# Kernel tuning notes

Hardware: AMD Instinct MI355X
Metric: run time of the kernel (lower is better)

## Reference

```python
import jax, jax.numpy as jnp
import numpy as np

R, N, E, F, D, A = 3, 50000, 800000, 128, 128, 64
EPS = 1e-5


def setup_inputs() -> dict:
    key = jax.random.key(0)
    ks = jax.random.split(key, 8)
    s = 0.05
    feat = jax.random.normal(ks[0], (N, F), jnp.float32)
    src = jax.random.randint(ks[1], (R, E), 0, N)
    dst = jax.random.randint(ks[2], (R, E), 0, N)
    W0 = jax.random.normal(ks[3], (R, F, D), jnp.float32) * s
    b0 = jnp.zeros((R, D), jnp.float32)
    W1 = jax.random.normal(ks[4], (R, D, D), jnp.float32) * s
    b1 = jnp.zeros((R, D), jnp.float32)
    ln_g = jnp.ones((R, D), jnp.float32)   # per-relation MessageTransform LayerNorm (shared across its 2 layers)
    ln_b = jnp.zeros((R, D), jnp.float32)
    LN_g = jnp.ones((D,), jnp.float32)     # final PROVGEM layer_norm
    LN_b = jnp.zeros((D,), jnp.float32)
    Wa1 = jax.random.normal(ks[5], (R, D, A), jnp.float32) * s  # semantic attention proj
    Wa2 = jax.random.normal(ks[6], (R, A), jnp.float32) * s     # semantic attention score vec
    return dict(feat=feat, src=src, dst=dst, W0=W0, b0=b0, W1=W1, b1=b1,
                ln_g=ln_g, ln_b=ln_b, LN_g=LN_g, LN_b=LN_b, Wa1=Wa1, Wa2=Wa2)


def _ln(x, g, b):
    mu = jnp.mean(x, axis=-1, keepdims=True)
    var = jnp.mean(jnp.square(x - mu), axis=-1, keepdims=True)
    return (x - mu) * jax.lax.rsqrt(var + EPS) * g + b


def _mean_agg(feat, src_r, dst_r):
    # copy_u + mean: gather source feats along edges, segment-mean into dst nodes
    msg = feat[src_r]                                            # [E, F]
    ssum = jax.ops.segment_sum(msg, dst_r, num_segments=N)       # [N, F]
    deg = jax.ops.segment_sum(jnp.ones((E,), feat.dtype), dst_r, num_segments=N)
    return ssum / jnp.maximum(deg, 1.0)[:, None]                 # 0 for zero-degree nodes


def reference(feat, src, dst, W0, b0, W1, b1, ln_g, ln_b, LN_g, LN_b, Wa1, Wa2):
    # per-relation aggregation (loop over small fixed R=3)
    neigh = jnp.stack([_mean_agg(feat, src[r], dst[r]) for r in range(R)])  # [R, N, F]
    h = feat[None, :, :] + neigh                                            # residual add
    x = jnp.einsum('rnf,rfd->rnd', h, W0) + b0[:, None, :]
    x = jax.nn.relu(_ln(x, ln_g[:, None, :], ln_b[:, None, :]))
    x = jnp.einsum('rnd,rde->rne', x, W1) + b1[:, None, :]
    x = jax.nn.relu(_ln(x, ln_g[:, None, :], ln_b[:, None, :]))
    # final LayerNorm over [R, N, D]
    h = _ln(x, LN_g, LN_b)
    # semantic attention over relations
    e = jnp.einsum('rna,ra->rn', jnp.tanh(jnp.einsum('rnd,rda->rna', h, Wa1)), Wa2)
    attn = jax.nn.softmax(e, axis=0)                                        # softmax over relations
    return jnp.einsum('rn,rnd->nd', attn, h)                                # [N, D]
```

## Files before the change

kernel.cpp:

```cpp
#include <hip/hip_runtime.h>

#define RR 3
#define NN 50000
#define EE 800000
#define FF 128
#define DD 128
#define AA 64
#define EPSF 1e-5f
#define RN (RR * NN)
#define RE (RR * EE)
#define NTPR ((NN + 127) / 128)
#define NBK (RR * NTPR)
#define ECHUNK 8192
#define NEBLK ((RE + ECHUNK - 1) / ECHUNK)
#define NTILES (NN / 16)

typedef __attribute__((ext_vector_type(8))) short bf16x8;
typedef __attribute__((ext_vector_type(4))) float f32x4;
typedef __attribute__((ext_vector_type(2))) float f32x2;

__device__ __forceinline__ short f2bs(float x) {
    union { float f; unsigned u; } v; v.f = x;
    unsigned rr = (v.u + 0x7fffu + ((v.u >> 16) & 1u)) >> 16;
    return (short)(rr & 0xffffu);
}

__device__ __forceinline__ float bs2f_lo(int p) {
    union { unsigned u; float f; } v; v.u = (unsigned)p << 16; return v.f;
}
__device__ __forceinline__ float bs2f_hi(int p) {
    union { unsigned u; float f; } v; v.u = (unsigned)p & 0xffff0000u; return v.f;
}

__device__ __forceinline__ int rel_of(long e) {
    return (e >= 2L * EE) ? 2 : ((e >= (long)EE) ? 1 : 0);
}

__device__ __forceinline__ float ftanh(float x) {
    float a = __expf(2.0f * fabsf(x));
    return copysignf(1.0f - 2.0f / (a + 1.0f), x);
}

__global__ __launch_bounds__(256)
void feat2both(const float* __restrict__ feat, short* __restrict__ featb,
               int* __restrict__ featq) {
    int gid = blockIdx.x * blockDim.x + threadIdx.x;
    if (gid >= NN * 16) return;
    f32x4 a = ((const f32x4*)feat)[2 * gid];
    f32x4 b = ((const f32x4*)feat)[2 * gid + 1];
    bf16x8 o;
    o[0] = f2bs(a.x); o[1] = f2bs(a.y); o[2] = f2bs(a.z); o[3] = f2bs(a.w);
    o[4] = f2bs(b.x); o[5] = f2bs(b.y); o[6] = f2bs(b.z); o[7] = f2bs(b.w);
    ((bf16x8*)featb)[gid] = o;
    int lo = 0, hi = 0;
    lo = __builtin_amdgcn_cvt_pk_fp8_f32(a.x, a.y, lo, false);
    lo = __builtin_amdgcn_cvt_pk_fp8_f32(a.z, a.w, lo, true);
    hi = __builtin_amdgcn_cvt_pk_fp8_f32(b.x, b.y, hi, false);
    hi = __builtin_amdgcn_cvt_pk_fp8_f32(b.z, b.w, hi, true);
    int2 pk; pk.x = lo; pk.y = hi;
    ((int2*)featq)[gid] = pk;
}

__global__ __launch_bounds__(256)
void count_kernel(const int* __restrict__ dst, int* __restrict__ bcnt) {
    __shared__ int hist[NBK];
    for (int i = threadIdx.x; i < NBK; i += 256) hist[i] = 0;
    __syncthreads();
    long ebase = (long)blockIdx.x * ECHUNK;
    for (int i = threadIdx.x; i < ECHUNK; i += 256) {
        long e = ebase + i;
        if (e < RE)
            atomicAdd(&hist[rel_of(e) * NTPR + (dst[e] >> 7)], 1);
    }
    __syncthreads();
    for (int i = threadIdx.x; i < NBK; i += 256) {
        int v = hist[i];
        if (v) atomicAdd(&bcnt[i], v);
    }
}

__global__ __launch_bounds__(256)
void bscan_kernel(const int* __restrict__ bcnt, int* __restrict__ bstart,
                  int* __restrict__ boff) {
    __shared__ int sm[256];
    int t = threadIdx.x;
    int loc[5];
    int s = 0;
    #pragma unroll
    for (int i = 0; i < 5; ++i) {
        int idx = t * 5 + i;
        int v = (idx < NBK) ? bcnt[idx] : 0;
        loc[i] = v; s += v;
    }
    sm[t] = s;
    __syncthreads();
    for (int d = 1; d < 256; d <<= 1) {
        int u = (t >= d) ? sm[t - d] : 0;
        __syncthreads();
        sm[t] += u;
        __syncthreads();
    }
    int run = sm[t] - s;
    #pragma unroll
    for (int i = 0; i < 5; ++i) {
        int idx = t * 5 + i;
        if (idx < NBK) { bstart[idx] = run; boff[idx] = run; run += loc[i]; }
    }
}

__global__ __launch_bounds__(256)
void bscatterA(const int* __restrict__ src, const int* __restrict__ dst,
               int* __restrict__ boff, unsigned* __restrict__ bpair) {
    __shared__ int hist[NBK];
    __shared__ int base[NBK];
    for (int i = threadIdx.x; i < NBK; i += 256) hist[i] = 0;
    __syncthreads();
    long ebase = (long)blockIdx.x * ECHUNK;
    for (int i = threadIdx.x; i < ECHUNK; i += 256) {
        long e = ebase + i;
        if (e < RE)
            atomicAdd(&hist[rel_of(e) * NTPR + (dst[e] >> 7)], 1);
    }
    __syncthreads();
    for (int i = threadIdx.x; i < NBK; i += 256) {
        int v = hist[i];
        base[i] = v ? atomicAdd(&boff[i], v) : 0;
    }
    __syncthreads();
    for (int i = threadIdx.x; i < ECHUNK; i += 256) {
        long e = ebase + i;
        if (e < RE) {
            int r = rel_of(e);
            int d = dst[e];
            int b = r * NTPR + (d >> 7);
            int pos = atomicAdd(&base[b], 1);
            bpair[pos] = ((unsigned)(d & 127) << 16) | (unsigned)src[e];
        }
    }
}

__global__ __launch_bounds__(256)
void scatterB(const unsigned* __restrict__ bpair, const int* __restrict__ bstart,
              const int* __restrict__ bcnt,
              int* __restrict__ off, int* __restrict__ cnt,
              int* __restrict__ csr) {
    __shared__ int hist[128];
    __shared__ int pre[128];
    __shared__ int base[128];
    int b = blockIdx.x;
    int r = b / NTPR, tile = b - r * NTPR;
    const int t = threadIdx.x;
    if (t < 128) hist[t] = 0;
    __syncthreads();
    int start = bstart[b], end = start + bcnt[b];
    for (int i = start + t; i < end; i += 256)
        atomicAdd(&hist[bpair[i] >> 16], 1);
    __syncthreads();
    if (t < 128) pre[t] = hist[t];
    __syncthreads();
    for (int d = 1; d < 128; d <<= 1) {
        int v = (t < 128 && t >= d) ? pre[t - d] : 0;
        __syncthreads();
        if (t < 128) pre[t] += v;
        __syncthreads();
    }
    if (t < 128) {
        int excl = pre[t] - hist[t];
        base[t] = start + excl;
        int nloc = tile * 128 + t;
        if (nloc < NN) {
            off[r * NN + nloc] = start + excl;
            cnt[r * NN + nloc] = hist[t];
        }
        hist[t] = 0;
    }
    __syncthreads();
    for (int i = start + t; i < end; i += 256) {
        unsigned p = bpair[i];
        int d = (int)(p >> 16);
        int rank = atomicAdd(&hist[d], 1);
        csr[base[d] + rank] = (int)(p & 0xFFFFu);
    }
}

__global__ __launch_bounds__(256)
void gather_kernel(const short* __restrict__ featb,
                   const int* __restrict__ featq,
                   const int* __restrict__ csr,
                   const int* __restrict__ off,
                   const int* __restrict__ cnt,
                   short* __restrict__ ssumb) {
    int gid = blockIdx.x * blockDim.x + threadIdx.x;
    int w = gid >> 6, lane = gid & 63;
    if (w >= RN) return;
    int c = cnt[w];
    int start = off[w];
    int end = start + c;
    const unsigned short* q = (const unsigned short*)featq;
    float ax0 = 0.f, ay0 = 0.f, ax1 = 0.f, ay1 = 0.f;
    float ax2 = 0.f, ay2 = 0.f, ax3 = 0.f, ay3 = 0.f;
    float ax4 = 0.f, ay4 = 0.f, ax5 = 0.f, ay5 = 0.f;
    float ax6 = 0.f, ay6 = 0.f, ax7 = 0.f, ay7 = 0.f;
    int j = start;
    for (; j + 7 < end; j += 8) {
        int s0 = csr[j + 0], s1 = csr[j + 1], s2 = csr[j + 2], s3 = csr[j + 3];
        int s4 = csr[j + 4], s5 = csr[j + 5], s6 = csr[j + 6], s7 = csr[j + 7];
        int v0 = q[(size_t)s0 * 64 + lane];
        int v1 = q[(size_t)s1 * 64 + lane];
        int v2 = q[(size_t)s2 * 64 + lane];
        int v3 = q[(size_t)s3 * 64 + lane];
        int v4 = q[(size_t)s4 * 64 + lane];
        int v5 = q[(size_t)s5 * 64 + lane];
        int v6 = q[(size_t)s6 * 64 + lane];
        int v7 = q[(size_t)s7 * 64 + lane];
        f32x2 f0 = __builtin_amdgcn_cvt_pk_f32_fp8(v0, false);
        f32x2 f1 = __builtin_amdgcn_cvt_pk_f32_fp8(v1, false);
        f32x2 f2v = __builtin_amdgcn_cvt_pk_f32_fp8(v2, false);
        f32x2 f3 = __builtin_amdgcn_cvt_pk_f32_fp8(v3, false);
        f32x2 f4 = __builtin_amdgcn_cvt_pk_f32_fp8(v4, false);
        f32x2 f5 = __builtin_amdgcn_cvt_pk_f32_fp8(v5, false);
        f32x2 f6 = __builtin_amdgcn_cvt_pk_f32_fp8(v6, false);
        f32x2 f7 = __builtin_amdgcn_cvt_pk_f32_fp8(v7, false);
        ax0 += f0[0]; ay0 += f0[1];
        ax1 += f1[0]; ay1 += f1[1];
        ax2 += f2v[0]; ay2 += f2v[1];
        ax3 += f3[0]; ay3 += f3[1];
        ax4 += f4[0]; ay4 += f4[1];
        ax5 += f5[0]; ay5 += f5[1];
        ax6 += f6[0]; ay6 += f6[1];
        ax7 += f7[0]; ay7 += f7[1];
    }
    for (; j + 3 < end; j += 4) {
        int s0 = csr[j + 0], s1 = csr[j + 1], s2 = csr[j + 2], s3 = csr[j + 3];
        int v0 = q[(size_t)s0 * 64 + lane];
        int v1 = q[(size_t)s1 * 64 + lane];
        int v2 = q[(size_t)s2 * 64 + lane];
        int v3 = q[(size_t)s3 * 64 + lane];
        f32x2 f0 = __builtin_amdgcn_cvt_pk_f32_fp8(v0, false);
        f32x2 f1 = __builtin_amdgcn_cvt_pk_f32_fp8(v1, false);
        f32x2 f2v = __builtin_amdgcn_cvt_pk_f32_fp8(v2, false);
        f32x2 f3 = __builtin_amdgcn_cvt_pk_f32_fp8(v3, false);
        ax0 += f0[0]; ay0 += f0[1];
        ax1 += f1[0]; ay1 += f1[1];
        ax2 += f2v[0]; ay2 += f2v[1];
        ax3 += f3[0]; ay3 += f3[1];
    }
    for (; j < end; ++j) {
        int s = csr[j];
        int v = q[(size_t)s * 64 + lane];
        f32x2 f0 = __builtin_amdgcn_cvt_pk_f32_fp8(v, false);
        ax0 += f0[0]; ay0 += f0[1];
    }
    float ax = ((ax0 + ax1) + (ax2 + ax3)) + ((ax4 + ax5) + (ax6 + ax7));
    float ay = ((ay0 + ay1) + (ay2 + ay3)) + ((ay4 + ay5) + (ay6 + ay7));
    float inv = 1.0f / fmaxf((float)c, 1.0f);
    int n = w % NN;
    int fv = ((const int*)featb)[(size_t)n * 64 + lane];
    float hx = bs2f_lo(fv) + ax * inv;
    float hy = bs2f_hi(fv) + ay * inv;
    unsigned plo = (unsigned short)f2bs(hx);
    unsigned phi = (unsigned short)f2bs(hy);
    ((int*)ssumb)[(size_t)w * 64 + lane] = (int)((phi << 16) | plo);
}


__device__ __forceinline__ void mfma_layer(const bf16x8 A[4], const short* Wlds,
                                           int g8, int c, f32x4 acc[8]) {
    #pragma unroll
    for (int kk = 0; kk < 4; ++kk) {
        #pragma unroll
        for (int t = 0; t < 8; ++t) {
            int d = t * 16 + c;
            bf16x8 B = *(const bf16x8*)&Wlds[d * 128 + ((kk * 32 + g8) ^ ((d & 7) << 3))];
            acc[t] = __builtin_amdgcn_mfma_f32_16x16x32_bf16(A[kk], B, acc[t], 0, 0, 0);
        }
    }
}

template <bool RELU, bool BIAS>
__device__ __forceinline__ void ln_block(f32x4 acc[8], const float* bias,
                                         const float* gam, const float* bet, int c) {
    float s0 = 0, s1 = 0, s2 = 0, s3 = 0, p0 = 0, p1 = 0, p2 = 0, p3 = 0;
    #pragma unroll
    for (int t = 0; t < 8; ++t) {
        if (BIAS) {
            float bb = bias[t * 16 + c];
            acc[t][0] += bb; acc[t][1] += bb;
            acc[t][2] += bb; acc[t][3] += bb;
        }
        s0 += acc[t][0]; p0 += acc[t][0] * acc[t][0];
        s1 += acc[t][1]; p1 += acc[t][1] * acc[t][1];
        s2 += acc[t][2]; p2 += acc[t][2] * acc[t][2];
        s3 += acc[t][3]; p3 += acc[t][3] * acc[t][3];
    }
    #pragma unroll
    for (int m = 1; m < 16; m <<= 1) {
        s0 += __shfl_xor(s0, m); s1 += __shfl_xor(s1, m);
        s2 += __shfl_xor(s2, m); s3 += __shfl_xor(s3, m);
        p0 += __shfl_xor(p0, m); p1 += __shfl_xor(p1, m);
        p2 += __shfl_xor(p2, m); p3 += __shfl_xor(p3, m);
    }
    const float inv = 1.0f / 128.0f;
    float mu0 = s0 * inv, mu1 = s1 * inv, mu2 = s2 * inv, mu3 = s3 * inv;
    float r0 = rsqrtf(p0 * inv - mu0 * mu0 + EPSF);
    float r1 = rsqrtf(p1 * inv - mu1 * mu1 + EPSF);
    float r2 = rsqrtf(p2 * inv - mu2 * mu2 + EPSF);
    float r3 = rsqrtf(p3 * inv - mu3 * mu3 + EPSF);
    #pragma unroll
    for (int t = 0; t < 8; ++t) {
        float gg = gam[t * 16 + c], bb = bet[t * 16 + c];
        float v0 = (acc[t][0] - mu0) * r0 * gg + bb;
        float v1 = (acc[t][1] - mu1) * r1 * gg + bb;
        float v2 = (acc[t][2] - mu2) * r2 * gg + bb;
        float v3 = (acc[t][3] - mu3) * r3 * gg + bb;
        if (RELU) {
            v0 = fmaxf(v0, 0.f); v1 = fmaxf(v1, 0.f);
            v2 = fmaxf(v2, 0.f); v3 = fmaxf(v3, 0.f);
        }
        acc[t][0] = v0; acc[t][1] = v1;
        acc[t][2] = v2; acc[t][3] = v3;
    }
}

__device__ __forceinline__ void store_ht(const f32x4 acc[8], short* myht, int g, int c) {
    #pragma unroll
    for (int t = 0; t < 8; ++t) {
        int col = t * 16 + c;
        #pragma unroll
        for (int qq = 0; qq < 4; ++qq) {
            int row = g * 4 + qq;
            myht[row * 128 + (col ^ ((row & 7) << 3))] = f2bs(acc[t][qq]);
        }
    }
}

__device__ __forceinline__ void ht_to_global(const short* myht, short* gout, int g, int c) {
    #pragma unroll
    for (int cc = 0; cc < 4; ++cc) {
        int row = cc * 4 + g;
        int col0 = c * 8;
        bf16x8 v = *(const bf16x8*)&myht[row * 128 + (col0 ^ ((row & 7) << 3))];
        *(bf16x8*)&gout[row * FF + col0] = v;
    }
}

__global__ __launch_bounds__(512)
void fused_l1(short* hbuf,
              const float* __restrict__ W0, const float* __restrict__ b0,
              const float* __restrict__ ln_g, const float* __restrict__ ln_b) {
    __shared__ short W0t[FF * DD];
    __shared__ short ht[8][16 * DD];
    __shared__ float b0s[DD], lgs[DD], lbs[DD];

    const int r = blockIdx.y;
    const int tid = threadIdx.x;

    for (int i = tid; i < FF * DD; i += 512) {
        int k = i >> 7, d = i & 127;
        W0t[d * 128 + (k ^ ((d & 7) << 3))] = f2bs(W0[(size_t)r * FF * DD + i]);
    }
    if (tid < DD) {
        b0s[tid] = b0[r * DD + tid];
        lgs[tid] = ln_g[r * DD + tid];
        lbs[tid] = ln_b[r * DD + tid];
    }
    __syncthreads();

    const int wv = tid >> 6, ln = tid & 63;
    const int g = ln >> 4, c = ln & 15;
    const int g8 = g * 8;
    short* myht = ht[wv];

    for (int tile = blockIdx.x * 8 + wv; tile < NTILES; tile += gridDim.x * 8) {
        const int nbase = tile * 16;
        bf16x8 A[4];
        {
            const short* sp = hbuf + ((size_t)r * NN + nbase + c) * FF;
            #pragma unroll
            for (int kk = 0; kk < 4; ++kk)
                A[kk] = *(const bf16x8*)(sp + kk * 32 + g8);
        }
        f32x4 acc[8];
        #pragma unroll
        for (int t = 0; t < 8; ++t) acc[t] = (f32x4){0.f, 0.f, 0.f, 0.f};
        mfma_layer(A, W0t, g8, c, acc);
        ln_block<true, true>(acc, b0s, lgs, lbs, c);
        store_ht(acc, myht, g, c);
        ht_to_global(myht, hbuf + ((size_t)r * NN + nbase) * FF, g, c);
    }
}

__global__ __launch_bounds__(512)
void fused_l2(short* hbuf,
              const float* __restrict__ W1, const float* __restrict__ b1,
              const float* __restrict__ ln_g, const float* __restrict__ ln_b,
              const float* __restrict__ LN_g, const float* __restrict__ LN_b) {
    __shared__ short W1t[DD * DD];
    __shared__ short ht[8][16 * DD];
    __shared__ float b1s[DD], lgs[DD], lbs[DD], Lgs[DD], Lbs[DD];

    const int r = blockIdx.y;
    const int tid = threadIdx.x;

    for (int i = tid; i < DD * DD; i += 512) {
        int k = i >> 7, d = i & 127;
        W1t[d * 128 + (k ^ ((d & 7) << 3))] = f2bs(W1[(size_t)r * DD * DD + i]);
    }
    if (tid < DD) {
        b1s[tid] = b1[r * DD + tid];
        lgs[tid] = ln_g[r * DD + tid];
        lbs[tid] = ln_b[r * DD + tid];
        Lgs[tid] = LN_g[tid];
        Lbs[tid] = LN_b[tid];
    }
    __syncthreads();

    const int wv = tid >> 6, ln = tid & 63;
    const int g = ln >> 4, c = ln & 15;
    const int g8 = g * 8;
    short* myht = ht[wv];

    for (int tile = blockIdx.x * 8 + wv; tile < NTILES; tile += gridDim.x * 8) {
        const int nbase = tile * 16;
        bf16x8 A[4];
        {
            const short* sp = hbuf + ((size_t)r * NN + nbase + c) * FF;
            #pragma unroll
            for (int kk = 0; kk < 4; ++kk)
                A[kk] = *(const bf16x8*)(sp + kk * 32 + g8);
        }
        f32x4 acc[8];
        #pragma unroll
        for (int t = 0; t < 8; ++t) acc[t] = (f32x4){0.f, 0.f, 0.f, 0.f};
        mfma_layer(A, W1t, g8, c, acc);
        ln_block<true, true>(acc, b1s, lgs, lbs, c);
        ln_block<false, false>(acc, nullptr, Lgs, Lbs, c);
        store_ht(acc, myht, g, c);
        ht_to_global(myht, hbuf + ((size_t)r * NN + nbase) * FF, g, c);
    }
}

__global__ __launch_bounds__(256)
void attn_combine(const short* __restrict__ hbuf,
                  const float* __restrict__ Wa1, const float* __restrict__ Wa2,
                  float* __restrict__ out) {
    __shared__ short Wa1t[RR][AA * DD];
    __shared__ float wa2s[RR][AA];

    const int tid = threadIdx.x;
    for (int i = tid; i < RR * DD * AA; i += 256) {
        int r2 = i >> 13;
        int rem = i & 8191;
        int k = rem >> 6, a = rem & 63;
        Wa1t[r2][a * 128 + (k ^ ((a & 7) << 3))] = f2bs(Wa1[i]);
    }
    if (tid < RR * AA) wa2s[tid >> 6][tid & 63] = Wa2[tid];
    __syncthreads();

    const int wv = tid >> 6, ln = tid & 63;
    const int col = ln & 15, g = ln >> 4;
    const int g8 = g * 8, g4 = g * 4;

    for (int tile = blockIdx.x * 4 + wv; tile < NTILES; tile += gridDim.x * 4) {
        const int nbase = tile * 16;
        bf16x8 Bh[RR][4];
        float e[RR];
        #pragma unroll
        for (int r = 0; r < RR; ++r) {
            const short* hrow = hbuf + ((size_t)r * NN + nbase + col) * FF;
            #pragma unroll
            for (int kk = 0; kk < 4; ++kk)
                Bh[r][kk] = *(const bf16x8*)(hrow + kk * 32 + g8);
            f32x4 acc[4];
            #pragma unroll
            for (int t = 0; t < 4; ++t) acc[t] = (f32x4){0.f, 0.f, 0.f, 0.f};
            #pragma unroll
            for (int kk = 0; kk < 4; ++kk)
                #pragma unroll
                for (int t = 0; t < 4; ++t) {
                    int a_ = t * 16 + col;
                    bf16x8 Wf = *(const bf16x8*)&Wa1t[r][a_ * 128 + ((kk * 32 + g8) ^ ((a_ & 7) << 3))];
                    acc[t] = __builtin_amdgcn_mfma_f32_16x16x32_bf16(Wf, Bh[r][kk], acc[t], 0, 0, 0);
                }
            float ee = 0.f;
            #pragma unroll
            for (int t = 0; t < 4; ++t) {
                f32x4 wv2 = *(const f32x4*)&wa2s[r][t * 16 + g4];
                ee += ftanh(acc[t][0]) * wv2[0] + ftanh(acc[t][1]) * wv2[1]
                    + ftanh(acc[t][2]) * wv2[2] + ftanh(acc[t][3]) * wv2[3];
            }
            ee += __shfl_xor(ee, 16);
            ee += __shfl_xor(ee, 32);
            e[r] = ee;
        }
        float m = fmaxf(e[0], fmaxf(e[1], e[2]));
        float w0 = __expf(e[0] - m), w1 = __expf(e[1] - m), w2 = __expf(e[2] - m);
        float inv = 1.0f / (w0 + w1 + w2);
        w0 *= inv; w1 *= inv; w2 *= inv;

        float* orow = out + (size_t)(nbase + col) * DD;
        #pragma unroll
        for (int kk = 0; kk < 4; ++kk) {
            union { bf16x8 v; int i[4]; } u0, u1, u2;
            u0.v = Bh[0][kk]; u1.v = Bh[1][kk]; u2.v = Bh[2][kk];
            f32x4 lo, hi;
            #pragma unroll
            for (int p = 0; p < 4; ++p) {
                float va = w0 * bs2f_lo(u0.i[p]) + w1 * bs2f_lo(u1.i[p]) + w2 * bs2f_lo(u2.i[p]);
                float vb = w0 * bs2f_hi(u0.i[p]) + w1 * bs2f_hi(u1.i[p]) + w2 * bs2f_hi(u2.i[p]);
                if (p < 2) { lo[2 * p] = va; lo[2 * p + 1] = vb; }
                else       { hi[2 * (p - 2)] = va; hi[2 * (p - 2) + 1] = vb; }
            }
            *(f32x4*)(orow + kk * 32 + g8) = lo;
            *(f32x4*)(orow + kk * 32 + g8 + 4) = hi;
        }
    }
}

extern "C" void kernel_launch(void* const* d_in, const int* in_sizes, int n_in,
                              void* d_out, int out_size, void* d_ws, size_t ws_size,
                              hipStream_t stream) {
    const float* feat = (const float*)d_in[0];
    const int*   src  = (const int*)d_in[1];
    const int*   dst  = (const int*)d_in[2];
    const float* W0   = (const float*)d_in[3];
    const float* b0   = (const float*)d_in[4];
    const float* W1   = (const float*)d_in[5];
    const float* b1   = (const float*)d_in[6];
    const float* ln_g = (const float*)d_in[7];
    const float* ln_b = (const float*)d_in[8];
    const float* LN_g = (const float*)d_in[9];
    const float* LN_b = (const float*)d_in[10];
    const float* Wa1  = (const float*)d_in[11];
    const float* Wa2  = (const float*)d_in[12];
    float* out = (float*)d_out;

    short*    ssumb  = (short*)d_ws;
    short*    featb  = ssumb + (size_t)RN * FF;
    int*      featq  = (int*)(featb + (size_t)NN * FF);
    int*      cnt    = featq + (size_t)NN * 32;
    int*      off    = cnt + RN;
    int*      csr    = off + RN;
    int*      bcnt   = csr + RE;
    int*      bstart = bcnt + NBK;
    int*      boff   = bstart + NBK;
    unsigned* bpair  = (unsigned*)(boff + NBK);

    feat2both<<<(NN * 16 + 255) / 256, 256, 0, stream>>>(feat, featb, featq);
    hipMemsetAsync(bcnt, 0, (size_t)NBK * sizeof(int), stream);
    count_kernel<<<NEBLK, 256, 0, stream>>>(dst, bcnt);
    bscan_kernel<<<1, 256, 0, stream>>>(bcnt, bstart, boff);
    bscatterA<<<NEBLK, 256, 0, stream>>>(src, dst, boff, bpair);
    scatterB<<<NBK, 256, 0, stream>>>(bpair, bstart, bcnt, off, cnt, csr);
    gather_kernel<<<(RN * 64 + 255) / 256, 256, 0, stream>>>(featb, featq, csr, off, cnt, ssumb);

    const int GX = (NTILES + 7) / 8;
    fused_l1<<<dim3(GX, RR), 512, 0, stream>>>(ssumb, W0, b0, ln_g, ln_b);
    fused_l2<<<dim3(GX, RR), 512, 0, stream>>>(ssumb, W1, b1, ln_g, ln_b, LN_g, LN_b);
    attn_combine<<<(NTILES + 3) / 4, 256, 0, stream>>>(ssumb, Wa1, Wa2, out);
}
```

Baseline: 318.3 us.

## Split attention into per-relation score kernel and separate combine kernel

```diff
diff --git a/kernel.cpp b/kernel.cpp
--- a/kernel.cpp
+++ b/kernel.cpp
@@ -441,9 +441,9 @@
 }
 
 __global__ __launch_bounds__(256)
-void attn_combine(const short* __restrict__ hbuf,
-                  const float* __restrict__ Wa1, const float* __restrict__ Wa2,
-                  float* __restrict__ out) {
+void attn_score(const short* __restrict__ hbuf,
+                const float* __restrict__ Wa1, const float* __restrict__ Wa2,
+                float* __restrict__ evec) {
     __shared__ short Wa1t[RR][AA * DD];
     __shared__ float wa2s[RR][AA];
 
@@ -461,60 +461,58 @@
     const int col = ln & 15, g = ln >> 4;
     const int g8 = g * 8, g4 = g * 4;
 
-    for (int tile = blockIdx.x * 4 + wv; tile < NTILES; tile += gridDim.x * 4) {
-        const int nbase = tile * 16;
-        bf16x8 Bh[RR][4];
-        float e[RR];
-        #pragma unroll
-        for (int r = 0; r < RR; ++r) {
-            const short* hrow = hbuf + ((size_t)r * NN + nbase + col) * FF;
-            #pragma unroll
-            for (int kk = 0; kk < 4; ++kk)
-                Bh[r][kk] = *(const bf16x8*)(hrow + kk * 32 + g8);
-            f32x4 acc[4];
-            #pragma unroll
-            for (int t = 0; t < 4; ++t) acc[t] = (f32x4){0.f, 0.f, 0.f, 0.f};
-            #pragma unroll
-            for (int kk = 0; kk < 4; ++kk)
-                #pragma unroll
-                for (int t = 0; t < 4; ++t) {
-                    int a_ = t * 16 + col;
-                    bf16x8 Wf = *(const bf16x8*)&Wa1t[r][a_ * 128 + ((kk * 32 + g8) ^ ((a_ & 7) << 3))];
-                    acc[t] = __builtin_amdgcn_mfma_f32_16x16x32_bf16(Wf, Bh[r][kk], acc[t], 0, 0, 0);
-                }
-            float ee = 0.f;
+    for (int idx = blockIdx.x * 4 + wv; idx < RR * NTILES; idx += gridDim.x * 4) {
+        int r = idx / NTILES;
+        int tile = idx - r * NTILES;
+        int nbase = tile * 16;
+        const short* hrow = hbuf + ((size_t)r * NN + nbase + col) * FF;
+
+        f32x4 acc[4];
+        #pragma unroll
+        for (int t = 0; t < 4; ++t) acc[t] = (f32x4){0.f, 0.f, 0.f, 0.f};
+        #pragma unroll
+        for (int kk = 0; kk < 4; ++kk) {
+            bf16x8 Bh = *(const bf16x8*)(hrow + kk * 32 + g8);
             #pragma unroll
             for (int t = 0; t < 4; ++t) {
-                f32x4 wv2 = *(const f32x4*)&wa2s[r][t * 16 + g4];
-                ee += ftanh(acc[t][0]) * wv2[0] + ftanh(acc[t][1]) * wv2[1]
-                    + ftanh(acc[t][2]) * wv2[2] + ftanh(acc[t][3]) * wv2[3];
+                int a_ = t * 16 + col;
+                bf16x8 Wf = *(const bf16x8*)&Wa1t[r][a_ * 128 + ((kk * 32 + g8) ^ ((a_ & 7) << 3))];
+                acc[t] = __builtin_amdgcn_mfma_f32_16x16x32_bf16(Wf, Bh, acc[t], 0, 0, 0);
             }
-            ee += __shfl_xor(ee, 16);
-            ee += __shfl_xor(ee, 32);
-            e[r] = ee;
-        }
-        float m = fmaxf(e[0], fmaxf(e[1], e[2]));
-        float w0 = __expf(e[0] - m), w1 = __expf(e[1] - m), w2 = __expf(e[2] - m);
-        float inv = 1.0f / (w0 + w1 + w2);
-        w0 *= inv; w1 *= inv; w2 *= inv;
-
-        float* orow = out + (size_t)(nbase + col) * DD;
-        #pragma unroll
-        for (int kk = 0; kk < 4; ++kk) {
-            union { bf16x8 v; int i[4]; } u0, u1, u2;
-            u0.v = Bh[0][kk]; u1.v = Bh[1][kk]; u2.v = Bh[2][kk];
-            f32x4 lo, hi;
-            #pragma unroll
-            for (int p = 0; p < 4; ++p) {
-                float va = w0 * bs2f_lo(u0.i[p]) + w1 * bs2f_lo(u1.i[p]) + w2 * bs2f_lo(u2.i[p]);
-                float vb = w0 * bs2f_hi(u0.i[p]) + w1 * bs2f_hi(u1.i[p]) + w2 * bs2f_hi(u2.i[p]);
-                if (p < 2) { lo[2 * p] = va; lo[2 * p + 1] = vb; }
-                else       { hi[2 * (p - 2)] = va; hi[2 * (p - 2) + 1] = vb; }
-            }
-            *(f32x4*)(orow + kk * 32 + g8) = lo;
-            *(f32x4*)(orow + kk * 32 + g8 + 4) = hi;
-        }
-    }
+        }
+        float e = 0.f;
+        #pragma unroll
+        for (int t = 0; t < 4; ++t) {
+            f32x4 wv2 = *(const f32x4*)&wa2s[r][t * 16 + g4];
+            e += ftanh(acc[t][0]) * wv2[0] + ftanh(acc[t][1]) * wv2[1]
+               + ftanh(acc[t][2]) * wv2[2] + ftanh(acc[t][3]) * wv2[3];
+        }
+        e += __shfl_xor(e, 16);
+        e += __shfl_xor(e, 32);
+        if (ln < 16) evec[(size_t)r * NN + nbase + ln] = e;
+    }
+}
+
+__global__ __launch_bounds__(256)
+void combine_kernel(const short* __restrict__ hfb,
+                    const float* __restrict__ evec,
+                    float* __restrict__ out) {
+    int gid = blockIdx.x * blockDim.x + threadIdx.x;
+    if (gid >= NN * 64) return;
+    int n = gid >> 6, j = gid & 63;
+    float e0 = evec[n], e1 = evec[NN + n], e2 = evec[2 * NN + n];
+    float m = fmaxf(e0, fmaxf(e1, e2));
+    float w0 = __expf(e0 - m), w1 = __expf(e1 - m), w2 = __expf(e2 - m);
+    float inv = 1.0f / (w0 + w1 + w2);
+    w0 *= inv; w1 *= inv; w2 *= inv;
+    const int* h0 = (const int*)hfb + (size_t)n * 64;
+    const int* h1 = (const int*)hfb + ((size_t)NN + n) * 64;
+    const int* h2 = (const int*)hfb + ((size_t)2 * NN + n) * 64;
+    int a = h0[j], b = h1[j], d = h2[j];
+    float2 o;
+    o.x = w0 * bs2f_lo(a) + w1 * bs2f_lo(b) + w2 * bs2f_lo(d);
+    o.y = w0 * bs2f_hi(a) + w1 * bs2f_hi(b) + w2 * bs2f_hi(d);
+    ((float2*)out)[(size_t)n * 64 + j] = o;
 }
 
 extern "C" void kernel_launch(void* const* d_in, const int* in_sizes, int n_in,
@@ -541,7 +539,8 @@
     int*      cnt    = featq + (size_t)NN * 32;
     int*      off    = cnt + RN;
     int*      csr    = off + RN;
-    int*      bcnt   = csr + RE;
+    float*    evec   = (float*)(csr + RE);
+    int*      bcnt   = (int*)(evec + RN);
     int*      bstart = bcnt + NBK;
     int*      boff   = bstart + NBK;
     unsigned* bpair  = (unsigned*)(boff + NBK);
@@ -557,5 +556,6 @@
     const int GX = (NTILES + 7) / 8;
     fused_l1<<<dim3(GX, RR), 512, 0, stream>>>(ssumb, W0, b0, ln_g, ln_b);
     fused_l2<<<dim3(GX, RR), 512, 0, stream>>>(ssumb, W1, b1, ln_g, ln_b, LN_g, LN_b);
-    attn_combine<<<(NTILES + 3) / 4, 256, 0, stream>>>(ssumb, Wa1, Wa2, out);
-}
+    attn_score<<<512, 256, 0, stream>>>(ssumb, Wa1, Wa2, evec);
+    combine_kernel<<<(NN * 64 + 255) / 256, 256, 0, stream>>>(ssumb, evec, out);
+}
```

New measurement: 306.0 us. 1.04x faster.
